# Performance work log

Hardware: AMD Instinct MI355X
Metric: run time of the kernel (lower is better)

## Reference

```python
import jax, jax.numpy as jnp
import numpy as np

B, L, W = 4, 512, 256
VOCAB, E, H = 30000, 300, 768
N_LABELS = 6


def setup_inputs() -> dict:
    key = jax.random.key(0)
    ks = jax.random.split(key, 7)
    return {
        "word_seq": jax.random.randint(ks[0], (B, W), 0, VOCAB),
        "hidden_state": jax.random.normal(ks[1], (B, L, H), dtype=jnp.float32),
        "label_value_matrix": jax.random.randint(ks[2], (B, L, W), 0, N_LABELS),
        "emb_a": jax.random.normal(ks[3], (VOCAB, E), dtype=jnp.float32) * 0.02,
        "lin_w": jax.random.normal(ks[4], (E, H), dtype=jnp.float32) * 0.02,
        "lin_b": jax.random.normal(ks[5], (H,), dtype=jnp.float32) * 0.02,
        "emb_c": jax.random.normal(ks[6], (N_LABELS, H), dtype=jnp.float32) * 0.02,
    }


def reference(word_seq, hidden_state, label_value_matrix, emb_a, lin_w, lin_b, emb_c):
    temper = jnp.asarray(emb_c.shape[1], hidden_state.dtype) ** 0.5  # hidden_size ** 0.5
    # embedding_a lookup + linear projection: [B,W,E] -> [B,W,H]
    a = emb_a[word_seq] @ lin_w + lin_b
    # attention-style scores u = hidden_state @ a^T / temper : [B,L,W]
    u = jnp.einsum("blh,bwh->blw", hidden_state, a) / temper
    # masked exp-normalize WITHOUT max-subtraction (faithful to original)
    mask = jnp.clip(label_value_matrix, 0, 1).astype(u.dtype)
    delta_exp_u = jnp.exp(u) * mask
    p = delta_exp_u / (jnp.sum(delta_exp_u, axis=2, keepdims=True) + 1e-10)
    # embedding_c gather [B,L,W,H], weight by p and reduce over W -> [B,L,H]
    ec = emb_c[label_value_matrix]
    o = jnp.einsum("blw,blwh->blh", p, ec)
    return o
```

## Files before the change

### kernel.cpp

```cpp
#include <hip/hip_runtime.h>

#define BB 4
#define LL 512
#define WW 256
#define EE 300
#define HH 768

typedef __attribute__((ext_vector_type(8))) short bf16x8;
typedef __attribute__((ext_vector_type(4))) float f32x4;

__device__ __forceinline__ short f2bf(float f) {
    union { float f; unsigned u; } v; v.f = f;
    unsigned r = (v.u + 0x7FFFu + ((v.u >> 16) & 1u)) >> 16;
    return (short)r;
}

__global__ __launch_bounds__(256, 1) void k1_a_gemm(
    const int*   __restrict__ word_seq,
    const float* __restrict__ emb_a,
    const float* __restrict__ lin_w,
    const float* __restrict__ lin_b,
    short*       __restrict__ aT)
{
    __shared__ short eaL[2][64 * 168];
    __shared__ short lwL[2][64 * 168];

    const int t  = threadIdx.x;
    const int m0 = (blockIdx.x & 15) * 64;
    const int n0 = (blockIdx.x >> 4) * 64;

    const int lane = t & 63, wv = t >> 6;
    const int l15 = lane & 15, l4 = lane >> 4;

    const int r_ea = t >> 2;
    const int q_ea = t & 3;
    const int h_lw = t & 63;
    const int q_lw = t >> 6;

    const int  wrow    = word_seq[m0 + r_ea];
    const float* arow  = emb_a + (long)wrow * EE;

    f32x4 acc[4] = {};

    float ea_reg[40], lw_reg[40];

#pragma unroll
    for (int half = 0; half < 2; ++half) {
        const int k0 = half * 160;
        {
            const int cbase = k0 + q_ea * 40;
#pragma unroll
            for (int c4 = 0; c4 < 10; ++c4) {
                const int col = cbase + c4 * 4;
                if (col <= 296) {
                    const float4 p = *(const float4*)(arow + col);
                    ea_reg[c4 * 4 + 0] = p.x; ea_reg[c4 * 4 + 1] = p.y;
                    ea_reg[c4 * 4 + 2] = p.z; ea_reg[c4 * 4 + 3] = p.w;
                } else {
                    ea_reg[c4 * 4 + 0] = 0.f; ea_reg[c4 * 4 + 1] = 0.f;
                    ea_reg[c4 * 4 + 2] = 0.f; ea_reg[c4 * 4 + 3] = 0.f;
                }
            }
            const int cb2 = k0 + q_lw * 40;
#pragma unroll
            for (int j = 0; j < 40; ++j) {
                const int col = cb2 + j;
                lw_reg[j] = (col < EE) ? lin_w[(long)col * HH + n0 + h_lw] : 0.f;
            }
        }
        {
            const int eoff = r_ea * 168 + q_ea * 40;
#pragma unroll
            for (int c8 = 0; c8 < 5; ++c8) {
                bf16x8 sv;
#pragma unroll
                for (int j = 0; j < 8; ++j) sv[j] = f2bf(ea_reg[c8 * 8 + j]);
                *(bf16x8*)(&eaL[half][eoff + c8 * 8]) = sv;
            }
            const int loff = h_lw * 168 + q_lw * 40;
#pragma unroll
            for (int c8 = 0; c8 < 5; ++c8) {
                bf16x8 sv;
#pragma unroll
                for (int j = 0; j < 8; ++j) sv[j] = f2bf(lw_reg[c8 * 8 + j]);
                *(bf16x8*)(&lwL[half][loff + c8 * 8]) = sv;
            }
        }
        __syncthreads();
#pragma unroll
        for (int ks = 0; ks < 5; ++ks) {
            const bf16x8 af =
                *(const bf16x8*)(&eaL[half][(wv * 16 + l15) * 168 + ks * 32 + l4 * 8]);
#pragma unroll
            for (int nf = 0; nf < 4; ++nf) {
                const bf16x8 bfv =
                    *(const bf16x8*)(&lwL[half][(nf * 16 + l15) * 168 + ks * 32 + l4 * 8]);
                acc[nf] = __builtin_amdgcn_mfma_f32_16x16x32_bf16(af, bfv, acc[nf], 0, 0, 0);
            }
        }
    }

    const int b1 = m0 >> 8;
#pragma unroll
    for (int nf = 0; nf < 4; ++nf) {
        const int h    = n0 + nf * 16 + l15;
        const float bv = lin_b[h];
        const long hbase = ((long)(b1 * 96 + (h >> 3)) * 256) * 8 + (h & 7);
#pragma unroll
        for (int i = 0; i < 4; ++i) {
            const int w = (m0 & 255) + wv * 16 + l4 * 4 + i;
            aT[hbase + (long)w * 8] = f2bf(acc[nf][i] + bv);
        }
    }
}

__global__ __launch_bounds__(256, 1) void k2_attn(
    const float* __restrict__ hidden,
    const int*   __restrict__ label,
    const short* __restrict__ aT,
    float*       __restrict__ s_part)
{
    __shared__ short hid[16 * 776];
    __shared__ float s_lds[4][16][5];

    const int t = threadIdx.x, lane = t & 63, wv = t >> 6;
    const int l15 = lane & 15, l4 = lane >> 4;
    const int blt   = blockIdx.x >> 1;
    const int whalf = blockIdx.x & 1;
    const int bl0   = blt * 16;
    const int b     = bl0 >> 9;
    const int w0    = whalf * 128;

    {
        const float* hrow = hidden + (long)bl0 * HH;
#pragma unroll
        for (int j = 0; j < 6; ++j) {
            const int idx = (t + j * 256) * 8;
            const int row = idx / HH;
            const int col = idx - row * HH;
            const float4 p0 = *(const float4*)(hrow + idx);
            const float4 p1 = *(const float4*)(hrow + idx + 4);
            bf16x8 v;
            v[0] = f2bf(p0.x); v[1] = f2bf(p0.y); v[2] = f2bf(p0.z); v[3] = f2bf(p0.w);
            v[4] = f2bf(p1.x); v[5] = f2bf(p1.y); v[6] = f2bf(p1.z); v[7] = f2bf(p1.w);
            *(bf16x8*)(&hid[row * 776 + col]) = v;
        }
    }
    __syncthreads();

    const short* abase = aT + (long)b * 96 * 256 * 8;
    f32x4 acc[2] = {};

#pragma unroll
    for (int ks = 0; ks < 24; ++ks) {
        const bf16x8 af = *(const bf16x8*)(&hid[l15 * 776 + ks * 32 + l4 * 8]);
#pragma unroll
        for (int nf = 0; nf < 2; ++nf) {
            const int w = w0 + wv * 32 + nf * 16 + l15;
            const bf16x8 bfv =
                *(const bf16x8*)(abase + ((long)(ks * 4 + l4) * 256 + w) * 8);
            acc[nf] = __builtin_amdgcn_mfma_f32_16x16x32_bf16(af, bfv, acc[nf], 0, 0, 0);
        }
    }

    const float inv_temper = 0.03608439182435161f;
    float s_loc[4][5];
#pragma unroll
    for (int i = 0; i < 4; ++i)
#pragma unroll
        for (int c = 0; c < 5; ++c) s_loc[i][c] = 0.f;

    const int* lab_base = label + (long)bl0 * WW;
#pragma unroll
    for (int nf = 0; nf < 2; ++nf) {
        const int w = w0 + wv * 32 + nf * 16 + l15;
#pragma unroll
        for (int i = 0; i < 4; ++i) {
            const int row = l4 * 4 + i;
            const int lv  = lab_base[row * WW + w];
            const float e = __expf(acc[nf][i] * inv_temper);
#pragma unroll
            for (int c = 1; c <= 5; ++c)
                s_loc[i][c - 1] += (lv == c) ? e : 0.f;
        }
    }
#pragma unroll
    for (int i = 0; i < 4; ++i) {
#pragma unroll
        for (int c = 0; c < 5; ++c) {
            float v = s_loc[i][c];
            v += __shfl_xor(v, 1);
            v += __shfl_xor(v, 2);
            v += __shfl_xor(v, 4);
            v += __shfl_xor(v, 8);
            s_loc[i][c] = v;
        }
    }
    if (l15 == 0) {
#pragma unroll
        for (int i = 0; i < 4; ++i)
#pragma unroll
            for (int c = 0; c < 5; ++c)
                s_lds[wv][l4 * 4 + i][c] = s_loc[i][c];
    }
    __syncthreads();
    if (t < 16) {
#pragma unroll
        for (int c = 0; c < 5; ++c) {
            const float s = s_lds[0][t][c] + s_lds[1][t][c] +
                            s_lds[2][t][c] + s_lds[3][t][c];
            s_part[(long)(bl0 + t) * 10 + whalf * 5 + c] = s;
        }
    }
}

__global__ __launch_bounds__(256, 1) void k3_out(
    const float* __restrict__ s_part,
    const float* __restrict__ emb_c,
    float*       __restrict__ out)
{
    const int t  = threadIdx.x;
    const int r0 = blockIdx.x * 8;

    float ecv[3][5];
#pragma unroll
    for (int q = 0; q < 3; ++q)
#pragma unroll
        for (int c = 0; c < 5; ++c)
            ecv[q][c] = emb_c[(c + 1) * HH + t + q * 256];

    for (int r = 0; r < 8; ++r) {
        const int row = r0 + r;
        float s[5], den = 1e-10f;
#pragma unroll
        for (int c = 0; c < 5; ++c) {
            s[c] = s_part[(long)row * 10 + c] + s_part[(long)row * 10 + 5 + c];
            den += s[c];
        }
        const float id = 1.0f / den;
        float* orow = out + (long)row * HH;
#pragma unroll
        for (int q = 0; q < 3; ++q) {
            const float v = s[0] * ecv[q][0] + s[1] * ecv[q][1] + s[2] * ecv[q][2] +
                            s[3] * ecv[q][3] + s[4] * ecv[q][4];
            orow[t + q * 256] = v * id;
        }
    }
}

extern "C" void kernel_launch(void* const* d_in, const int* in_sizes, int n_in,
                              void* d_out, int out_size, void* d_ws, size_t ws_size,
                              hipStream_t stream) {
    const int*   word_seq = (const int*)  d_in[0];
    const float* hidden   = (const float*)d_in[1];
    const int*   label    = (const int*)  d_in[2];
    const float* emb_a    = (const float*)d_in[3];
    const float* lin_w    = (const float*)d_in[4];
    const float* lin_b    = (const float*)d_in[5];
    const float* emb_c    = (const float*)d_in[6];
    float* out = (float*)d_out;

    short* aT     = (short*)d_ws;
    float* s_part = (float*)((char*)d_ws + 0x180000);

    k1_a_gemm<<<dim3(192), 256, 0, stream>>>(word_seq, emb_a, lin_w, lin_b, aT);
    k2_attn<<<dim3(256), 256, 0, stream>>>(hidden, label, aT, s_part);
    k3_out<<<dim3(256), 256, 0, stream>>>(s_part, emb_c, out);
}
```

Baseline: 24.13 us.

## Retile attention kernel to 32 rows x 64 cols with XCD-aware block mapping

The attention kernel now uses 512 threads per block, covering 32 L-rows by 64 W-columns, with one MFMA tile per wave. Blocks are mapped so that all blocks on an XCD share one batch, to improve L2 reuse of aT. The aT layout is padded (WP=264) to avoid cache or channel conflicts, and label loads are hoisted ahead of the barrier. The partial sums grow to four W-slices per row, so the output kernel reduces four partials and launches twice as many smaller blocks. Each block now converts twice as many hidden rows, and there is less MFMA work per wave to hide that latency.

```diff
diff --git a/kernel.cpp b/kernel.cpp
--- a/kernel.cpp
+++ b/kernel.cpp
@@ -3,6 +3,7 @@
 #define BB 4
 #define LL 512
 #define WW 256
+#define WP 264
 #define EE 300
 #define HH 768
 
@@ -15,7 +16,7 @@
     return (short)r;
 }
 
-__global__ __launch_bounds__(256, 1) void k1_a_gemm(
+__global__ __launch_bounds__(256, 1) void kA_a_gemm(
     const int*   __restrict__ word_seq,
     const float* __restrict__ emb_a,
     const float* __restrict__ lin_w,
@@ -37,11 +38,10 @@
     const int h_lw = t & 63;
     const int q_lw = t >> 6;
 
-    const int  wrow    = word_seq[m0 + r_ea];
-    const float* arow  = emb_a + (long)wrow * EE;
+    const int    wrow = word_seq[m0 + r_ea];
+    const float* arow = emb_a + (long)wrow * EE;
 
     f32x4 acc[4] = {};
-
     float ea_reg[40], lw_reg[40];
 
 #pragma unroll
@@ -105,7 +105,7 @@
     for (int nf = 0; nf < 4; ++nf) {
         const int h    = n0 + nf * 16 + l15;
         const float bv = lin_b[h];
-        const long hbase = ((long)(b1 * 96 + (h >> 3)) * 256) * 8 + (h & 7);
+        const long hbase = ((long)(b1 * 96 + (h >> 3)) * WP) * 8 + (h & 7);
 #pragma unroll
         for (int i = 0; i < 4; ++i) {
             const int w = (m0 & 255) + wv * 16 + l4 * 4 + i;
@@ -114,75 +114,68 @@
     }
 }
 
-__global__ __launch_bounds__(256, 1) void k2_attn(
+__global__ __launch_bounds__(512, 1) void kB_attn(
     const float* __restrict__ hidden,
     const int*   __restrict__ label,
     const short* __restrict__ aT,
     float*       __restrict__ s_part)
 {
-    __shared__ short hid[16 * 776];
-    __shared__ float s_lds[4][16][5];
+    __shared__ short hid[32 * 776];
+    __shared__ float s_lds[4][2][16][5];
 
     const int t = threadIdx.x, lane = t & 63, wv = t >> 6;
     const int l15 = lane & 15, l4 = lane >> 4;
-    const int blt   = blockIdx.x >> 1;
-    const int whalf = blockIdx.x & 1;
-    const int bl0   = blt * 16;
-    const int b     = bl0 >> 9;
-    const int w0    = whalf * 128;
+    const int mh = wv >> 2, wq = wv & 3;
+
+    const int bid = blockIdx.x;
+    const int xcd = bid & 7, j = bid >> 3;
+    const int b   = xcd >> 1;
+    const int lt  = j >> 1;
+    const int ws  = ((xcd & 1) << 1) | (j & 1);
+    const int row0 = b * 512 + lt * 32;
+    const int wg   = ws * 64 + wq * 16 + l15;
 
     {
-        const float* hrow = hidden + (long)bl0 * HH;
-#pragma unroll
-        for (int j = 0; j < 6; ++j) {
-            const int idx = (t + j * 256) * 8;
-            const int row = idx / HH;
-            const int col = idx - row * HH;
-            const float4 p0 = *(const float4*)(hrow + idx);
-            const float4 p1 = *(const float4*)(hrow + idx + 4);
+        const float* hrow = hidden + (long)row0 * HH;
+#pragma unroll
+        for (int jj = 0; jj < 6; ++jj) {
+            const int ci  = t + jj * 512;
+            const int row = ci / 96;
+            const int col = (ci - row * 96) * 8;
+            const float4 p0 = *(const float4*)(hrow + (long)row * HH + col);
+            const float4 p1 = *(const float4*)(hrow + (long)row * HH + col + 4);
             bf16x8 v;
             v[0] = f2bf(p0.x); v[1] = f2bf(p0.y); v[2] = f2bf(p0.z); v[3] = f2bf(p0.w);
             v[4] = f2bf(p1.x); v[5] = f2bf(p1.y); v[6] = f2bf(p1.z); v[7] = f2bf(p1.w);
             *(bf16x8*)(&hid[row * 776 + col]) = v;
         }
     }
+
+    int lv[4];
+#pragma unroll
+    for (int i = 0; i < 4; ++i)
+        lv[i] = label[((long)row0 + mh * 16 + l4 * 4 + i) * WW + wg];
     __syncthreads();
 
-    const short* abase = aT + (long)b * 96 * 256 * 8;
-    f32x4 acc[2] = {};
-
+    const short* abase = aT + (long)b * 96 * WP * 8;
+    f32x4 acc = {};
 #pragma unroll
     for (int ks = 0; ks < 24; ++ks) {
-        const bf16x8 af = *(const bf16x8*)(&hid[l15 * 776 + ks * 32 + l4 * 8]);
-#pragma unroll
-        for (int nf = 0; nf < 2; ++nf) {
-            const int w = w0 + wv * 32 + nf * 16 + l15;
-            const bf16x8 bfv =
-                *(const bf16x8*)(abase + ((long)(ks * 4 + l4) * 256 + w) * 8);
-            acc[nf] = __builtin_amdgcn_mfma_f32_16x16x32_bf16(af, bfv, acc[nf], 0, 0, 0);
-        }
+        const bf16x8 af =
+            *(const bf16x8*)(&hid[(mh * 16 + l15) * 776 + ks * 32 + l4 * 8]);
+        const bf16x8 bfv =
+            *(const bf16x8*)(abase + ((long)(ks * 4 + l4) * WP + wg) * 8);
+        acc = __builtin_amdgcn_mfma_f32_16x16x32_bf16(af, bfv, acc, 0, 0, 0);
     }
 
     const float inv_temper = 0.03608439182435161f;
     float s_loc[4][5];
 #pragma unroll
-    for (int i = 0; i < 4; ++i)
-#pragma unroll
-        for (int c = 0; c < 5; ++c) s_loc[i][c] = 0.f;
-
-    const int* lab_base = label + (long)bl0 * WW;
-#pragma unroll
-    for (int nf = 0; nf < 2; ++nf) {
-        const int w = w0 + wv * 32 + nf * 16 + l15;
-#pragma unroll
-        for (int i = 0; i < 4; ++i) {
-            const int row = l4 * 4 + i;
-            const int lv  = lab_base[row * WW + w];
-            const float e = __expf(acc[nf][i] * inv_temper);
-#pragma unroll
-            for (int c = 1; c <= 5; ++c)
-                s_loc[i][c - 1] += (lv == c) ? e : 0.f;
-        }
+    for (int i = 0; i < 4; ++i) {
+        const float e = __expf(acc[i] * inv_temper);
+#pragma unroll
+        for (int c = 1; c <= 5; ++c)
+            s_loc[i][c - 1] = (lv[i] == c) ? e : 0.f;
     }
 #pragma unroll
     for (int i = 0; i < 4; ++i) {
@@ -201,26 +194,26 @@
         for (int i = 0; i < 4; ++i)
 #pragma unroll
             for (int c = 0; c < 5; ++c)
-                s_lds[wv][l4 * 4 + i][c] = s_loc[i][c];
+                s_lds[wq][mh][l4 * 4 + i][c] = s_loc[i][c];
     }
     __syncthreads();
-    if (t < 16) {
+    if (t < 32) {
 #pragma unroll
         for (int c = 0; c < 5; ++c) {
-            const float s = s_lds[0][t][c] + s_lds[1][t][c] +
-                            s_lds[2][t][c] + s_lds[3][t][c];
-            s_part[(long)(bl0 + t) * 10 + whalf * 5 + c] = s;
-        }
-    }
-}
-
-__global__ __launch_bounds__(256, 1) void k3_out(
+            const float s = s_lds[0][t >> 4][t & 15][c] + s_lds[1][t >> 4][t & 15][c] +
+                            s_lds[2][t >> 4][t & 15][c] + s_lds[3][t >> 4][t & 15][c];
+            s_part[((long)row0 + t) * 20 + ws * 5 + c] = s;
+        }
+    }
+}
+
+__global__ __launch_bounds__(256) void k3_out(
     const float* __restrict__ s_part,
     const float* __restrict__ emb_c,
     float*       __restrict__ out)
 {
     const int t  = threadIdx.x;
-    const int r0 = blockIdx.x * 8;
+    const int r0 = blockIdx.x * 4;
 
     float ecv[3][5];
 #pragma unroll
@@ -229,12 +222,15 @@
         for (int c = 0; c < 5; ++c)
             ecv[q][c] = emb_c[(c + 1) * HH + t + q * 256];
 
-    for (int r = 0; r < 8; ++r) {
+#pragma unroll
+    for (int r = 0; r < 4; ++r) {
         const int row = r0 + r;
+        const long sb = (long)row * 20;
         float s[5], den = 1e-10f;
 #pragma unroll
         for (int c = 0; c < 5; ++c) {
-            s[c] = s_part[(long)row * 10 + c] + s_part[(long)row * 10 + 5 + c];
+            s[c] = s_part[sb + c] + s_part[sb + 5 + c] +
+                   s_part[sb + 10 + c] + s_part[sb + 15 + c];
             den += s[c];
         }
         const float id = 1.0f / den;
@@ -261,9 +257,9 @@
     float* out = (float*)d_out;
 
     short* aT     = (short*)d_ws;
-    float* s_part = (float*)((char*)d_ws + 0x180000);
-
-    k1_a_gemm<<<dim3(192), 256, 0, stream>>>(word_seq, emb_a, lin_w, lin_b, aT);
-    k2_attn<<<dim3(256), 256, 0, stream>>>(hidden, label, aT, s_part);
-    k3_out<<<dim3(256), 256, 0, stream>>>(s_part, emb_c, out);
-}
+    float* s_part = (float*)((char*)d_ws + 0x200000);
+
+    kA_a_gemm<<<dim3(192), 256, 0, stream>>>(word_seq, emb_a, lin_w, lin_b, aT);
+    kB_attn<<<dim3(256), 512, 0, stream>>>(hidden, label, aT, s_part);
+    k3_out<<<dim3(512), 256, 0, stream>>>(s_part, emb_c, out);
+}
```

Result: faster. 22.88 us (-5.2%).
